# Kernel optimization log

Measured on AMD Instinct MI355X. Metric: run time of the kernel, lower is better.

Reference implementation:

```python
import jax, jax.numpy as jnp
import numpy as np

N, K, C = 2, 512, 256
IMG = 1024.0
P = 7            # output_size
S = 2            # sampling_ratio
SCALES = (0.25, 0.125, 0.0625, 0.03125)
MIN_LEVEL, MAX_LEVEL = 2, 5
CANON_SIZE, CANON_LEVEL = 224.0, 4


def setup_inputs() -> dict:
    key = jax.random.key(0)
    ks = jax.random.split(key, 7)
    feats = {}
    for i, (hw, kk) in enumerate(zip((256, 128, 64, 32), ks[:4])):
        feats[f"feat{i + 2}"] = jax.random.normal(kk, (N, C, hw, hw), dtype=jnp.float32)
    # boxes: centers uniform in image, sizes log-uniform in [32, 512] px -> spans all levels
    cxy = jax.random.uniform(ks[4], (N, K, 2), minval=0.0, maxval=IMG)
    wh = 32.0 * jnp.exp2(jax.random.uniform(ks[5], (N, K, 2), minval=0.0, maxval=4.0))
    x1y1 = jnp.clip(cxy - wh / 2, 0.0, IMG)
    x2y2 = jnp.clip(cxy + wh / 2, 0.0, IMG)
    boxes = jnp.concatenate([x1y1, x2y2], axis=-1).astype(jnp.float32)  # [N,K,4] xyxy
    feats["boxes"] = boxes
    return feats


def _roi_align_level(feat, boxes, batch_idx, scale):
    """ROIAlignV2 (aligned=True). feat [N,C,H,W], boxes [M,4] xyxy in image coords."""
    Nf, Cf, H, W = feat.shape
    M = boxes.shape[0]
    b = boxes * scale - 0.5  # aligned=True shift
    x1, y1, x2, y2 = b[:, 0], b[:, 1], b[:, 2], b[:, 3]
    bin_h = (y2 - y1) / P
    bin_w = (x2 - x1) / P
    # combined bin+sample grid: coord = start + ((i + 0.5)/S) * bin, i in [0, P*S)
    g = (jnp.arange(P * S, dtype=feat.dtype) + 0.5) / S  # [PS]
    y = y1[:, None] + g[None, :] * bin_h[:, None]  # [M, PS]
    x = x1[:, None] + g[None, :] * bin_w[:, None]  # [M, PS]

    def prep(c, size):
        valid = (c >= -1.0) & (c <= size)
        c = jnp.maximum(c, 0.0)
        lo = jnp.minimum(jnp.floor(c).astype(jnp.int32), size - 1)
        hi = jnp.minimum(lo + 1, size - 1)
        frac = c - lo.astype(c.dtype)  # harmless if >1 when lo==hi==size-1
        return lo, hi, frac, valid

    yl, yh, fy, vy = prep(y, H)
    xl, xh, fx, vx = prep(x, W)
    bi = batch_idx[:, None, None]

    def gather(yy, xx):
        # -> [M, PS, PS, C]
        return feat[bi, :, yy[:, :, None], xx[:, None, :]]

    fy_ = fy[:, :, None, None]
    fx_ = fx[:, None, :, None]
    v = ((1 - fy_) * ((1 - fx_) * gather(yl, xl) + fx_ * gather(yl, xh))
         + fy_ * ((1 - fx_) * gather(yh, xl) + fx_ * gather(yh, xh)))
    mask = (vy[:, :, None] & vx[:, None, :])[..., None]
    v = jnp.where(mask, v, jnp.zeros((), feat.dtype))
    out = v.reshape(M, P, S, P, S, Cf).mean(axis=(2, 4))  # avg over sampling grid
    return out.transpose(0, 3, 1, 2)  # [M, C, P, P]


def reference(feat2, feat3, feat4, feat5, boxes):
    feats = [feat2, feat3, feat4, feat5]
    flat = boxes.reshape(-1, 4)  # [M,4], concat over images
    batch_idx = jnp.repeat(jnp.arange(N, dtype=jnp.int32), K)
    # assign_boxes_to_levels
    area = (flat[:, 2] - flat[:, 0]) * (flat[:, 3] - flat[:, 1])
    sizes = jnp.sqrt(area)
    lvl = jnp.floor(CANON_LEVEL + jnp.log2(sizes / CANON_SIZE + 1e-8))
    lvl = jnp.clip(lvl, MIN_LEVEL, MAX_LEVEL).astype(jnp.int32) - MIN_LEVEL  # [M] in 0..3
    out = jnp.zeros((flat.shape[0], C, P, P), dtype=feat2.dtype)
    for l, (feat, scale) in enumerate(zip(feats, SCALES)):
        o = _roi_align_level(feat, flat, batch_idx, scale)
        out = jnp.where((lvl == l)[:, None, None, None], o, out)
    return out
```

## Files before the change

kernel.cpp:

```cpp
#include <hip/hip_runtime.h>
#include <math.h>
#include <stdint.h>

#define NBATCH 2
#define KBOX   512
#define CCH    256
#define NBIN   49
#define NCH    8
#define BPB    (CCH/NCH)
#define COUT   (CCH*NBIN)
#define WCAP   1152

typedef const uint32_t __attribute__((address_space(1)))* gas_u32p;
typedef uint32_t       __attribute__((address_space(3)))* las_u32p;

__global__ __launch_bounds__(256, 4) void roi_align_kernel(
    const float* __restrict__ f2, const float* __restrict__ f3,
    const float* __restrict__ f4, const float* __restrict__ f5,
    const float* __restrict__ boxes, float* __restrict__ out)
{
    const int bid  = blockIdx.x;
    const int m    = bid >> 5;
    const int cg   = bid & 31;
    const int tid  = threadIdx.x;
    const int lane = tid & 63;
    const int wid  = tid >> 6;
    const int b    = m / KBOX;

    __shared__ float win[NCH * WCAP];

    const float x1 = boxes[m*4+0];
    const float y1 = boxes[m*4+1];
    const float x2 = boxes[m*4+2];
    const float y2 = boxes[m*4+3];

    const float area = (x2 - x1) * (y2 - y1);
    const float size = sqrtf(area);
    float lvlf = floorf(4.0f + log2f(size / 224.0f + 1e-8f));
    lvlf = fminf(fmaxf(lvlf, 2.0f), 5.0f);
    const int lvl = (int)lvlf - 2;

    const int   H     = 256 >> lvl;
    const int   HH    = H * H;
    const float scale = 0.25f / (float)(1 << lvl);
    const float Hf    = (float)H;

    const float* fptr = (lvl == 0) ? f2 : (lvl == 1) ? f3 : (lvl == 2) ? f4 : f5;
    const int c0 = cg * NCH;
    const float* plane0 = fptr + ((size_t)b * CCH + c0) * HH;

    const float bx1 = x1 * scale - 0.5f;
    const float by1 = y1 * scale - 0.5f;
    const float bin_w = (x2 * scale - 0.5f - bx1) / 7.0f;
    const float bin_h = (y2 * scale - 0.5f - by1) / 7.0f;

    const float sx_min = bx1 + 0.25f * bin_w;
    const float sx_max = bx1 + 6.75f * bin_w;
    const float sy_min = by1 + 0.25f * bin_h;
    const float sy_max = by1 + 6.75f * bin_h;
    const int wx0 = min((int)floorf(fmaxf(sx_min, 0.0f)), H - 1);
    const int wy0 = min((int)floorf(fmaxf(sy_min, 0.0f)), H - 1);
    const int wx1 = min(min((int)floorf(fmaxf(sx_max, 0.0f)), H - 1) + 1, H - 1);
    const int wy1 = min(min((int)floorf(fmaxf(sy_max, 0.0f)), H - 1) + 1, H - 1);
    const int wspan = wx1 - wx0 + 1;
    const int hspan = wy1 - wy0 + 1;
    const int wsz   = wspan * hspan;

    const float* src0 = plane0 + wy0 * H + wx0;
    for (int i = tid; i < wsz; i += 256) {
        const int r   = i / wspan;
        const int col = i - r * wspan;
        const float* sp = src0 + r * H + col;
        const int ldsbase = i & ~63;
        #pragma unroll
        for (int c = 0; c < NCH; ++c) {
            __builtin_amdgcn_global_load_lds(
                (gas_u32p)(const void*)(sp + (size_t)c * HH),
                (las_u32p)(void*)(&win[c * WCAP + ldsbase]),
                4, 0, 0);
        }
    }
    if (tid < NCH) win[tid * WCAP + wsz] = 0.0f;

    const int bin = (lane < 49) ? lane : 48;
    const int py  = bin / 7;
    const int px  = bin - py * 7;

    int   o8 [8];
    float wlo[8];
    float whi[8];
    #pragma unroll
    for (int s = 0; s < 4; ++s) {
        const int iy = s >> 1;
        const int ix = s & 1;
        const float gy = ((float)(2*py + iy) + 0.5f) * 0.5f;
        const float gx = ((float)(2*px + ix) + 0.5f) * 0.5f;
        const float yy = by1 + gy * bin_h;
        const float xx = bx1 + gx * bin_w;

        const bool valid = (yy >= -1.0f) && (yy <= Hf) && (xx >= -1.0f) && (xx <= Hf);

        const float yc = fmaxf(yy, 0.0f);
        const float xc = fmaxf(xx, 0.0f);
        int yl = min((int)floorf(yc), H - 1);
        int xl = min((int)floorf(xc), H - 1);
        const int yh = min(yl + 1, H - 1);
        const int xh = min(xl + 1, H - 1);
        const float fy = yc - (float)yl;
        float fx = xc - (float)xl;
        if (xh == xl) fx = 0.0f;

        const float vm  = valid ? 0.25f : 0.0f;
        const float wyl = (1.0f - fy) * vm;
        const float wyh = fy * vm;

        const int xr = xl - wx0;
        o8 [2*s  ] = (yl - wy0) * wspan + xr;
        o8 [2*s+1] = (yh - wy0) * wspan + xr;
        wlo[2*s  ] = wyl * (1.0f - fx);
        whi[2*s  ] = wyl * fx;
        wlo[2*s+1] = wyh * (1.0f - fx);
        whi[2*s+1] = wyh * fx;
    }

    __syncthreads();

    const float* wa = win + (wid * 2    ) * WCAP;
    const float* wb = win + (wid * 2 + 1) * WCAP;

    float acc0 = 0.0f, acc1 = 0.0f;
    #pragma unroll
    for (int j = 0; j < 8; ++j) {
        const int oj = o8[j];
        const float a_lo = wa[oj], a_hi = wa[oj + 1];
        const float b_lo = wb[oj], b_hi = wb[oj + 1];
        acc0 += wlo[j] * a_lo + whi[j] * a_hi;
        acc1 += wlo[j] * b_lo + whi[j] * b_hi;
    }

    if (lane < 49) {
        float* outp = out + (size_t)m * COUT + (size_t)(c0 + wid * 2) * NBIN + lane;
        __builtin_nontemporal_store(acc0, outp);
        __builtin_nontemporal_store(acc1, outp + NBIN);
    }
}

extern "C" void kernel_launch(void* const* d_in, const int* in_sizes, int n_in,
                              void* d_out, int out_size, void* d_ws, size_t ws_size,
                              hipStream_t stream) {
    const float* f2    = (const float*)d_in[0];
    const float* f3    = (const float*)d_in[1];
    const float* f4    = (const float*)d_in[2];
    const float* f5    = (const float*)d_in[3];
    const float* boxes = (const float*)d_in[4];
    float* outp = (float*)d_out;

    dim3 grid(NBATCH * KBOX * BPB);
    dim3 block(256);
    roi_align_kernel<<<grid, block, 0, stream>>>(f2, f3, f4, f5, boxes, outp);
}
```

Measured before the change: 105.1 us.

## Precompute per-box level, window and bilinear taps in a separate prep kernel

```diff
diff --git a/kernel.cpp b/kernel.cpp
--- a/kernel.cpp
+++ b/kernel.cpp
@@ -4,30 +4,24 @@
 
 #define NBATCH 2
 #define KBOX   512
+#define NBOX   (NBATCH*KBOX)
 #define CCH    256
 #define NBIN   49
 #define NCH    8
 #define BPB    (CCH/NCH)
 #define COUT   (CCH*NBIN)
 #define WCAP   1152
+#define HDRN   8
+#define TAPN   (24*NBIN)
 
 typedef const uint32_t __attribute__((address_space(1)))* gas_u32p;
 typedef uint32_t       __attribute__((address_space(3)))* las_u32p;
 
-__global__ __launch_bounds__(256, 4) void roi_align_kernel(
-    const float* __restrict__ f2, const float* __restrict__ f3,
-    const float* __restrict__ f4, const float* __restrict__ f5,
-    const float* __restrict__ boxes, float* __restrict__ out)
+__global__ __launch_bounds__(64) void box_prep_kernel(
+    const float* __restrict__ boxes, int* __restrict__ hdr, int* __restrict__ taps)
 {
-    const int bid  = blockIdx.x;
-    const int m    = bid >> 5;
-    const int cg   = bid & 31;
-    const int tid  = threadIdx.x;
-    const int lane = tid & 63;
-    const int wid  = tid >> 6;
-    const int b    = m / KBOX;
-
-    __shared__ float win[NCH * WCAP];
+    const int m    = blockIdx.x;
+    const int lane = threadIdx.x;
 
     const float x1 = boxes[m*4+0];
     const float y1 = boxes[m*4+1];
@@ -41,13 +35,8 @@
     const int lvl = (int)lvlf - 2;
 
     const int   H     = 256 >> lvl;
-    const int   HH    = H * H;
     const float scale = 0.25f / (float)(1 << lvl);
     const float Hf    = (float)H;
-
-    const float* fptr = (lvl == 0) ? f2 : (lvl == 1) ? f3 : (lvl == 2) ? f4 : f5;
-    const int c0 = cg * NCH;
-    const float* plane0 = fptr + ((size_t)b * CCH + c0) * HH;
 
     const float bx1 = x1 * scale - 0.5f;
     const float by1 = y1 * scale - 0.5f;
@@ -66,7 +55,89 @@
     const int hspan = wy1 - wy0 + 1;
     const int wsz   = wspan * hspan;
 
-    const float* src0 = plane0 + wy0 * H + wx0;
+    if (lane < NBIN) {
+        const int py = lane / 7;
+        const int px = lane - py * 7;
+        const int base = m * TAPN;
+        float* tapf = (float*)taps;
+
+        #pragma unroll
+        for (int s = 0; s < 4; ++s) {
+            const int iy = s >> 1;
+            const int ix = s & 1;
+            const float gy = ((float)(2*py + iy) + 0.5f) * 0.5f;
+            const float gx = ((float)(2*px + ix) + 0.5f) * 0.5f;
+            const float yy = by1 + gy * bin_h;
+            const float xx = bx1 + gx * bin_w;
+
+            const bool valid = (yy >= -1.0f) && (yy <= Hf) && (xx >= -1.0f) && (xx <= Hf);
+
+            const float yc = fmaxf(yy, 0.0f);
+            const float xc = fmaxf(xx, 0.0f);
+            int yl = min((int)floorf(yc), H - 1);
+            int xl = min((int)floorf(xc), H - 1);
+            const int yh = min(yl + 1, H - 1);
+            const int xh = min(xl + 1, H - 1);
+            const float fy = yc - (float)yl;
+            float fx = xc - (float)xl;
+            if (xh == xl) fx = 0.0f;
+
+            const float vm  = valid ? 0.25f : 0.0f;
+            const float wyl = (1.0f - fy) * vm;
+            const float wyh = fy * vm;
+
+            const int xr = xl - wx0;
+            const int o_lo = (yl - wy0) * wspan + xr;
+            const int o_hi = (yh - wy0) * wspan + xr;
+
+            taps[base + (2*s  )*NBIN + lane] = o_lo;
+            taps[base + (2*s+1)*NBIN + lane] = o_hi;
+            tapf[base + (8 + 2*s  )*NBIN + lane] = wyl * (1.0f - fx);
+            tapf[base + (8 + 2*s+1)*NBIN + lane] = wyh * (1.0f - fx);
+            tapf[base + (16 + 2*s  )*NBIN + lane] = wyl * fx;
+            tapf[base + (16 + 2*s+1)*NBIN + lane] = wyh * fx;
+        }
+    }
+
+    if (lane == 0) {
+        int* h = hdr + m * HDRN;
+        h[0] = lvl;
+        h[1] = H;
+        h[2] = H * H;
+        h[3] = wy0 * H + wx0;
+        h[4] = wspan;
+        h[5] = wsz;
+    }
+}
+
+__global__ __launch_bounds__(256, 4) void roi_align_kernel(
+    const float* __restrict__ f2, const float* __restrict__ f3,
+    const float* __restrict__ f4, const float* __restrict__ f5,
+    const int* __restrict__ hdr, const int* __restrict__ taps,
+    float* __restrict__ out)
+{
+    const int bid  = blockIdx.x;
+    const int m    = bid >> 5;
+    const int cg   = bid & 31;
+    const int tid  = threadIdx.x;
+    const int lane = tid & 63;
+    const int wid  = tid >> 6;
+    const int b    = m >> 9;
+
+    __shared__ float win[NCH * WCAP];
+
+    const int* h = hdr + m * HDRN;
+    const int lvl   = h[0];
+    const int H     = h[1];
+    const int HH    = h[2];
+    const int woff  = h[3];
+    const int wspan = h[4];
+    const int wsz   = h[5];
+
+    const float* fptr = (lvl == 0) ? f2 : (lvl == 1) ? f3 : (lvl == 2) ? f4 : f5;
+    const int c0 = cg * NCH;
+    const float* src0 = fptr + ((size_t)(b * CCH + c0)) * HH + woff;
+
     for (int i = tid; i < wsz; i += 256) {
         const int r   = i / wspan;
         const int col = i - r * wspan;
@@ -82,46 +153,19 @@
     }
     if (tid < NCH) win[tid * WCAP + wsz] = 0.0f;
 
-    const int bin = (lane < 49) ? lane : 48;
-    const int py  = bin / 7;
-    const int px  = bin - py * 7;
+    const int lidx = (lane < NBIN) ? lane : NBIN - 1;
+    const int tb = m * TAPN;
+    const float* tf = (const float*)taps;
 
     int   o8 [8];
     float wlo[8];
     float whi[8];
     #pragma unroll
-    for (int s = 0; s < 4; ++s) {
-        const int iy = s >> 1;
-        const int ix = s & 1;
-        const float gy = ((float)(2*py + iy) + 0.5f) * 0.5f;
-        const float gx = ((float)(2*px + ix) + 0.5f) * 0.5f;
-        const float yy = by1 + gy * bin_h;
-        const float xx = bx1 + gx * bin_w;
-
-        const bool valid = (yy >= -1.0f) && (yy <= Hf) && (xx >= -1.0f) && (xx <= Hf);
-
-        const float yc = fmaxf(yy, 0.0f);
-        const float xc = fmaxf(xx, 0.0f);
-        int yl = min((int)floorf(yc), H - 1);
-        int xl = min((int)floorf(xc), H - 1);
-        const int yh = min(yl + 1, H - 1);
-        const int xh = min(xl + 1, H - 1);
-        const float fy = yc - (float)yl;
-        float fx = xc - (float)xl;
-        if (xh == xl) fx = 0.0f;
-
-        const float vm  = valid ? 0.25f : 0.0f;
-        const float wyl = (1.0f - fy) * vm;
-        const float wyh = fy * vm;
-
-        const int xr = xl - wx0;
-        o8 [2*s  ] = (yl - wy0) * wspan + xr;
-        o8 [2*s+1] = (yh - wy0) * wspan + xr;
-        wlo[2*s  ] = wyl * (1.0f - fx);
-        whi[2*s  ] = wyl * fx;
-        wlo[2*s+1] = wyh * (1.0f - fx);
-        whi[2*s+1] = wyh * fx;
-    }
+    for (int j = 0; j < 8; ++j) o8 [j] = taps[tb + j*NBIN + lidx];
+    #pragma unroll
+    for (int j = 0; j < 8; ++j) wlo[j] = tf[tb + (8  + j)*NBIN + lidx];
+    #pragma unroll
+    for (int j = 0; j < 8; ++j) whi[j] = tf[tb + (16 + j)*NBIN + lidx];
 
     __syncthreads();
 
@@ -138,7 +182,7 @@
         acc1 += wlo[j] * b_lo + whi[j] * b_hi;
     }
 
-    if (lane < 49) {
+    if (lane < NBIN) {
         float* outp = out + (size_t)m * COUT + (size_t)(c0 + wid * 2) * NBIN + lane;
         __builtin_nontemporal_store(acc0, outp);
         __builtin_nontemporal_store(acc1, outp + NBIN);
@@ -155,7 +199,10 @@
     const float* boxes = (const float*)d_in[4];
     float* outp = (float*)d_out;
 
-    dim3 grid(NBATCH * KBOX * BPB);
-    dim3 block(256);
-    roi_align_kernel<<<grid, block, 0, stream>>>(f2, f3, f4, f5, boxes, outp);
+    int* hdr  = (int*)d_ws;
+    int* taps = (int*)d_ws + NBOX * HDRN;
+
+    box_prep_kernel<<<dim3(NBOX), dim3(64), 0, stream>>>(boxes, hdr, taps);
+    roi_align_kernel<<<dim3(NBOX * BPB), dim3(256), 0, stream>>>(
+        f2, f3, f4, f5, hdr, taps, outp);
 }
```

Result: slower. 112.7 us (+7.2%).
